# Performance work log

Measured on AMD Instinct MI355X. Metric: run time of the kernel, lower is better.

Reference implementation:

```python
import jax, jax.numpy as jnp
import numpy as np

N0, N1, N2, N3 = 262144, 65536, 16384, 4096
EPS = 1e-5  # BatchNorm1d default eps


def setup_inputs() -> dict:
    key = jax.random.key(0)
    ks = jax.random.split(key, 10)
    f0 = jax.random.normal(ks[0], (N0, 64), dtype=jnp.float32)
    f1 = jax.random.normal(ks[1], (N1, 128), dtype=jnp.float32)
    f2 = jax.random.normal(ks[2], (N2, 256), dtype=jnp.float32)
    f3 = jax.random.normal(ks[3], (N3, 512), dtype=jnp.float32)
    # upsampling indices: finer level gathers from coarser level
    idx0 = jax.random.randint(ks[4], (N2,), 0, N3, dtype=jnp.int32)   # f3 -> level2
    idx1 = jax.random.randint(ks[5], (N1,), 0, N2, dtype=jnp.int32)   # f2 -> level1
    idx2 = jax.random.randint(ks[6], (N0,), 0, N1, dtype=jnp.int32)   # f1 -> level0
    # BN weight init'd to constant 0.25 in the module; bias defaults to 0
    bn_w2, bn_b2 = jnp.full((512,), 0.25, jnp.float32), jnp.zeros((512,), jnp.float32)
    bn_w1, bn_b1 = jnp.full((256,), 0.25, jnp.float32), jnp.zeros((256,), jnp.float32)
    bn_w0, bn_b0 = jnp.full((128,), 0.25, jnp.float32), jnp.zeros((128,), jnp.float32)
    # Linear(in, out, bias=False) weights, torch layout [out, in]
    W2 = jax.random.normal(ks[7], (256, 512), dtype=jnp.float32) * 0.02
    W1 = jax.random.normal(ks[8], (128, 256), dtype=jnp.float32) * 0.02
    W0 = jax.random.normal(ks[9], (64, 128), dtype=jnp.float32) * 0.02
    return dict(f0=f0, f1=f1, f2=f2, f3=f3,
                bn_w2=bn_w2, bn_b2=bn_b2, W2=W2,
                bn_w1=bn_w1, bn_b1=bn_b1, W1=W1,
                bn_w0=bn_w0, bn_b0=bn_b0, W0=W0,
                idx0=idx0, idx1=idx1, idx2=idx2)


def _decode(f, bn_w, bn_b, W):
    # BatchNorm1d (training-mode batch stats, biased variance) -> Linear (no bias)
    mean = jnp.mean(f, axis=0)
    var = jnp.var(f, axis=0)
    xn = (f - mean) * jax.lax.rsqrt(var + EPS)
    return (xn * bn_w + bn_b) @ W.T  # [N, out_ch]


def reference(f0, f1, f2, f3, bn_w2, bn_b2, W2, bn_w1, bn_b1, W1,
              bn_w0, bn_b0, W0, idx0, idx1, idx2):
    # gather (upsample) -> BN -> Linear -> residual add, coarse to fine
    f2 = f2 + _decode(f3[idx0], bn_w2, bn_b2, W2)   # [N2, 256]
    f1 = f1 + _decode(f2[idx1], bn_w1, bn_b1, W1)   # [N1, 128]
    f0 = f0 + _decode(f1[idx2], bn_w0, bn_b0, W0)   # [N0, 64]
    return f0
```

## Files before the change

### kernel.cpp

```cpp
#include <hip/hip_runtime.h>
#include <hip/hip_cooperative_groups.h>

namespace cg = cooperative_groups;

#define BN_EPS 1e-5f

constexpr int PN0 = 262144, PN1 = 65536, PN2 = 16384, PN3 = 4096;
constexpr int NTHR = 512;
constexpr size_t MB = 1u << 20;

typedef __attribute__((ext_vector_type(8))) short short8;
typedef __attribute__((ext_vector_type(4))) float f32x4;
typedef __attribute__((ext_vector_type(4))) unsigned int u32x4;

__device__ __forceinline__ unsigned f2bf(float f) {
    unsigned u = __builtin_bit_cast(unsigned, f);
    u += 0x7fff + ((u >> 16) & 1);
    return u >> 16;
}
__device__ __forceinline__ float bf2f(unsigned h) {
    return __builtin_bit_cast(float, h << 16);
}
__device__ __forceinline__ f32x4 ntload4(const float* p) {
    return __builtin_nontemporal_load(reinterpret_cast<const f32x4*>(p));
}
__device__ __forceinline__ void ntstore4(float* p, f32x4 v) {
    __builtin_nontemporal_store(v, reinterpret_cast<f32x4*>(p));
}
#define SCHED_FENCE() __builtin_amdgcn_sched_barrier(0)

struct MegaArgs {
    const float *f0, *f1, *f2, *f3;
    const float *bnw2, *bnb2, *W2;
    const float *bnw1, *bnb1, *W1;
    const float *bnw0, *bnb0, *W0;
    const int *idx0, *idx1, *idx2;
    unsigned short *f3bf, *dec2, *dec1, *dec0, *f2p, *f1p;
    int *cnt2, *cnt1;
    float *part2, *part1, *part0;
    float *out;
};

template<int G, int NL>
__device__ __forceinline__ void red_write(float* aux, const float s[8], const float q[8],
                                          int t, int lr, int cgi,
                                          float* part, int vb, int C) {
    #pragma unroll
    for (int j = 0; j < 8; ++j) aux[(lr * G + cgi) * 8 + j] = s[j];
    __syncthreads();
    if (t < G) {
        float ss[8] = {};
        for (int l = 0; l < NL; ++l)
            #pragma unroll
            for (int j = 0; j < 8; ++j) ss[j] += aux[(l * G + t) * 8 + j];
        #pragma unroll
        for (int j = 0; j < 8; ++j)
            part[((size_t)vb * C + t * 8 + j) * 2] = ss[j];
    }
    __syncthreads();
    #pragma unroll
    for (int j = 0; j < 8; ++j) aux[(lr * G + cgi) * 8 + j] = q[j];
    __syncthreads();
    if (t < G) {
        float qq[8] = {};
        for (int l = 0; l < NL; ++l)
            #pragma unroll
            for (int j = 0; j < 8; ++j) qq[j] += aux[(l * G + t) * 8 + j];
        #pragma unroll
        for (int j = 0; j < 8; ++j)
            part[((size_t)vb * C + t * 8 + j) * 2 + 1] = qq[j];
    }
    __syncthreads();
}

__device__ void stats_gathered(const MegaArgs& a, int vb, int t, float* aux) {
    const int cgi = t & 63, lr = t >> 6;
    const int r0 = vb * 128;
    float s[8] = {}, q[8] = {};
    for (int ii = 0; ii < 4; ++ii) {
        int gi[8];
        #pragma unroll
        for (int j = 0; j < 8; ++j) gi[j] = a.idx0[r0 + lr + 4 * (ii * 8 + j)];
        float4 x0[8], x1[8];
        #pragma unroll
        for (int j = 0; j < 8; ++j) {
            const float* p = a.f3 + (size_t)gi[j] * 512 + cgi * 8;
            x0[j] = *reinterpret_cast<const float4*>(p);
            x1[j] = *reinterpret_cast<const float4*>(p + 4);
        }
        SCHED_FENCE();
        #pragma unroll
        for (int j = 0; j < 8; ++j) {
            float v[8] = {x0[j].x, x0[j].y, x0[j].z, x0[j].w,
                          x1[j].x, x1[j].y, x1[j].z, x1[j].w};
            #pragma unroll
            for (int k = 0; k < 8; ++k) { s[k] += v[k]; q[k] += v[k] * v[k]; }
        }
    }
    red_write<64, 4>(aux, s, q, t, lr, cgi, a.part2, vb, 512);
}

__device__ void cvt_f3(const MegaArgs& a, int vb, int t) {
    const int cgi = t & 63, lr = t >> 6;
    const int r0 = vb * 32;
    float4 x0[8], x1[8];
    #pragma unroll
    for (int i = 0; i < 8; ++i) {
        const float* p = a.f3 + (size_t)(r0 + lr + 4 * i) * 512 + cgi * 8;
        x0[i] = *reinterpret_cast<const float4*>(p);
        x1[i] = *reinterpret_cast<const float4*>(p + 4);
    }
    SCHED_FENCE();
    #pragma unroll
    for (int i = 0; i < 8; ++i) {
        uint4 o;
        o.x = f2bf(x0[i].x) | (f2bf(x0[i].y) << 16);
        o.y = f2bf(x0[i].z) | (f2bf(x0[i].w) << 16);
        o.z = f2bf(x1[i].x) | (f2bf(x1[i].y) << 16);
        o.w = f2bf(x1[i].z) | (f2bf(x1[i].w) << 16);
        *reinterpret_cast<uint4*>(a.f3bf + (size_t)(r0 + lr + 4 * i) * 512 + cgi * 8) = o;
    }
}

__device__ void phase1(const MegaArgs& a, int nbv, int vb0, int t, float* aux) {
    for (int vb = vb0; vb < 416; vb += nbv) {
        if (vb < 128) {
            stats_gathered(a, vb, t, aux);
        } else if (vb < 256) {
            cvt_f3(a, vb - 128, t);
        } else if (vb < 288) {
            int b = vb - 256;
            int v[8];
            #pragma unroll
            for (int i = 0; i < 8; ++i) v[i] = a.idx1[b * 2048 + i * 256 + t];
            SCHED_FENCE();
            #pragma unroll
            for (int i = 0; i < 8; ++i) atomicAdd(&a.cnt2[v[i]], 1);
        } else {
            int b = vb - 288;
            int v[8];
            #pragma unroll
            for (int i = 0; i < 8; ++i) v[i] = a.idx2[b * 2048 + i * 256 + t];
            SCHED_FENCE();
            #pragma unroll
            for (int i = 0; i < 8; ++i) atomicAdd(&a.cnt1[v[i]], 1);
        }
    }
}

template<int K, int NB>
__device__ void calc_scsh(int tid, const float* part, const float* bnw, const float* bnb,
                          float invN, float* sc, float* sh) {
    for (int c = tid; c < K; c += NTHR) {
        float s = 0.f, q = 0.f;
        for (int b = 0; b < NB; ++b) {
            float2 p = *reinterpret_cast<const float2*>(part + ((size_t)b * K + c) * 2);
            s += p.x;
            q += p.y;
        }
        float mean = s * invN;
        float var = fmaxf(q * invN - mean * mean, 0.f);
        float scl = bnw[c] * rsqrtf(var + BN_EPS);
        sc[c] = scl;
        sh[c] = bnb[c] - mean * scl;
    }
    __syncthreads();
}

__device__ void g2_phase(const MegaArgs& a, int nb, int bid, int tid,
                         unsigned short* Wl, float* sc, float* sh, float* dl) {
    constexpr int K = 512;
    calc_scsh<512, 128>(tid, a.part2, a.bnw2, a.bnb2, 1.f / PN2, sc, sh);
    const int lane = tid & 63;
    const int w = tid >> 6;
    const int l15 = lane & 15, lg = lane >> 4;
    const int n32 = tid >> 4, kc = tid & 15;

    for (int vb = bid; vb < 256; vb += nb) {
        const int chunk = vb & 31, panel = vb >> 5;
        const int row = chunk * 128 + w * 16 + l15;
        const unsigned short* xp = a.f3bf + (size_t)row * K + lg * 8;
        short8 xf[16];
        #pragma unroll
        for (int kk = 0; kk < 16; ++kk)
            xf[kk] = *reinterpret_cast<const short8*>(xp + kk * 32);

        {
            const float* wrow = a.W2 + (size_t)(panel * 32 + n32) * K;
            float dp = 0.f;
            #pragma unroll
            for (int i = 0; i < 4; ++i) {
                int k = kc * 32 + i * 8;
                float4 w0 = *reinterpret_cast<const float4*>(wrow + k);
                float4 w1 = *reinterpret_cast<const float4*>(wrow + k + 4);
                float4 s0 = *reinterpret_cast<const float4*>(&sc[k]);
                float4 s1 = *reinterpret_cast<const float4*>(&sc[k + 4]);
                float4 h0 = *reinterpret_cast<const float4*>(&sh[k]);
                float4 h1 = *reinterpret_cast<const float4*>(&sh[k + 4]);
                dp += h0.x * w0.x + h0.y * w0.y + h0.z * w0.z + h0.w * w0.w
                    + h1.x * w1.x + h1.y * w1.y + h1.z * w1.z + h1.w * w1.w;
                uint4 o;
                o.x = f2bf(w0.x * s0.x) | (f2bf(w0.y * s0.y) << 16);
                o.y = f2bf(w0.z * s0.z) | (f2bf(w0.w * s0.w) << 16);
                o.z = f2bf(w1.x * s1.x) | (f2bf(w1.y * s1.y) << 16);
                o.w = f2bf(w1.z * s1.z) | (f2bf(w1.w * s1.w) << 16);
                int si = (n32 * K + k) ^ ((n32 & 7) << 3);
                *reinterpret_cast<uint4*>(&Wl[si]) = o;
            }
            dp += __shfl_xor(dp, 1); dp += __shfl_xor(dp, 2);
            dp += __shfl_xor(dp, 4); dp += __shfl_xor(dp, 8);
            if (kc == 0) dl[n32] = dp;
        }
        __syncthreads();

        f32x4 acc[2];
        acc[0] = (f32x4){0.f, 0.f, 0.f, 0.f};
        acc[1] = (f32x4){0.f, 0.f, 0.f, 0.f};
        #pragma unroll
        for (int kk = 0; kk < 16; ++kk) {
            #pragma unroll
            for (int ni = 0; ni < 2; ++ni) {
                const int si = ((ni * 16 + l15) * K + kk * 32 + lg * 8) ^ ((l15 & 7) << 3);
                short8 wf = *reinterpret_cast<const short8*>(&Wl[si]);
                acc[ni] = __builtin_amdgcn_mfma_f32_16x16x32_bf16(wf, xf[kk], acc[ni], 0, 0, 0);
            }
        }

        const size_t rowoff = (size_t)row * 256 + panel * 32;
        #pragma unroll
        for (int ni = 0; ni < 2; ++ni) {
            float4 dr = *reinterpret_cast<const float4*>(&dl[ni * 16 + lg * 4]);
            size_t off = rowoff + ni * 16 + lg * 4;
            float v0 = dr.x + acc[ni][0];
            float v1 = dr.y + acc[ni][1];
            float v2 = dr.z + acc[ni][2];
            float v3 = dr.w + acc[ni][3];
            *reinterpret_cast<uint2*>(&a.dec2[off]) =
                make_uint2(f2bf(v0) | (f2bf(v1) << 16), f2bf(v2) | (f2bf(v3) << 16));
        }
        __syncthreads();
    }
}

__device__ void g1_phase(const MegaArgs& a, int nb, int bid, int tid,
                         unsigned short* Wl, float* sc, float* sh, float* dl) {
    constexpr int K = 256;
    calc_scsh<256, 256>(tid, a.part1, a.bnw1, a.bnb1, 1.f / PN1, sc, sh);
    const int lane = tid & 63;
    const int w = tid >> 6;
    const int l15 = lane & 15, lg = lane >> 4;
    const int n = tid >> 3, kc = tid & 7;

    for (int vb = bid; vb < 256; vb += nb) {
        const int chunk = vb & 127, panel = vb >> 7;
        const int row = chunk * 128 + w * 16 + l15;
        const unsigned short* xp = a.f2p + (size_t)row * K + lg * 8;
        short8 xf[8];
        #pragma unroll
        for (int kk = 0; kk < 8; ++kk)
            xf[kk] = *reinterpret_cast<const short8*>(xp + kk * 32);

        {
            const float* wrow = a.W1 + (size_t)(panel * 64 + n) * K;
            float dp = 0.f;
            #pragma unroll
            for (int i = 0; i < 4; ++i) {
                int k = kc * 32 + i * 8;
                float4 w0 = *reinterpret_cast<const float4*>(wrow + k);
                float4 w1 = *reinterpret_cast<const float4*>(wrow + k + 4);
                float4 s0 = *reinterpret_cast<const float4*>(&sc[k]);
                float4 s1 = *reinterpret_cast<const float4*>(&sc[k + 4]);
                float4 h0 = *reinterpret_cast<const float4*>(&sh[k]);
                float4 h1 = *reinterpret_cast<const float4*>(&sh[k + 4]);
                dp += h0.x * w0.x + h0.y * w0.y + h0.z * w0.z + h0.w * w0.w
                    + h1.x * w1.x + h1.y * w1.y + h1.z * w1.z + h1.w * w1.w;
                uint4 o;
                o.x = f2bf(w0.x * s0.x) | (f2bf(w0.y * s0.y) << 16);
                o.y = f2bf(w0.z * s0.z) | (f2bf(w0.w * s0.w) << 16);
                o.z = f2bf(w1.x * s1.x) | (f2bf(w1.y * s1.y) << 16);
                o.w = f2bf(w1.z * s1.z) | (f2bf(w1.w * s1.w) << 16);
                int si = (n * K + k) ^ ((n & 7) << 3);
                *reinterpret_cast<uint4*>(&Wl[si]) = o;
            }
            dp += __shfl_xor(dp, 1); dp += __shfl_xor(dp, 2); dp += __shfl_xor(dp, 4);
            if (kc == 0) dl[n] = dp;
        }
        __syncthreads();

        f32x4 acc[4];
        #pragma unroll
        for (int ni = 0; ni < 4; ++ni) acc[ni] = (f32x4){0.f, 0.f, 0.f, 0.f};
        #pragma unroll
        for (int kk = 0; kk < 8; ++kk) {
            #pragma unroll
            for (int ni = 0; ni < 4; ++ni) {
                const int si = ((ni * 16 + l15) * K + kk * 32 + lg * 8) ^ ((l15 & 7) << 3);
                short8 wf = *reinterpret_cast<const short8*>(&Wl[si]);
                acc[ni] = __builtin_amdgcn_mfma_f32_16x16x32_bf16(wf, xf[kk], acc[ni], 0, 0, 0);
            }
        }

        const size_t rowoff = (size_t)row * 128 + panel * 64;
        #pragma unroll
        for (int ni = 0; ni < 4; ++ni) {
            float4 dr = *reinterpret_cast<const float4*>(&dl[ni * 16 + lg * 4]);
            size_t off = rowoff + ni * 16 + lg * 4;
            float v0 = dr.x + acc[ni][0];
            float v1 = dr.y + acc[ni][1];
            float v2 = dr.z + acc[ni][2];
            float v3 = dr.w + acc[ni][3];
            *reinterpret_cast<uint2*>(&a.dec1[off]) =
                make_uint2(f2bf(v0) | (f2bf(v1) << 16), f2bf(v2) | (f2bf(v3) << 16));
        }
        __syncthreads();
    }
}

__device__ void g0_phase(const MegaArgs& a, int nb, int bid, int tid,
                         unsigned short* Wl, float* sc, float* sh, float* dl) {
    constexpr int K = 128;
    calc_scsh<128, 512>(tid, a.part0, a.bnw0, a.bnb0, 1.f / PN0, sc, sh);
    const int lane = tid & 63;
    const int w = tid >> 6;
    const int l15 = lane & 15, lg = lane >> 4;
    const int n = tid >> 3, kc = tid & 7;

    {
        const float* wrow = a.W0 + (size_t)n * K;
        float dp = 0.f;
        #pragma unroll
        for (int i = 0; i < 2; ++i) {
            int k = kc * 16 + i * 8;
            float4 w0 = *reinterpret_cast<const float4*>(wrow + k);
            float4 w1 = *reinterpret_cast<const float4*>(wrow + k + 4);
            float4 s0 = *reinterpret_cast<const float4*>(&sc[k]);
            float4 s1 = *reinterpret_cast<const float4*>(&sc[k + 4]);
            float4 h0 = *reinterpret_cast<const float4*>(&sh[k]);
            float4 h1 = *reinterpret_cast<const float4*>(&sh[k + 4]);
            dp += h0.x * w0.x + h0.y * w0.y + h0.z * w0.z + h0.w * w0.w
                + h1.x * w1.x + h1.y * w1.y + h1.z * w1.z + h1.w * w1.w;
            uint4 o;
            o.x = f2bf(w0.x * s0.x) | (f2bf(w0.y * s0.y) << 16);
            o.y = f2bf(w0.z * s0.z) | (f2bf(w0.w * s0.w) << 16);
            o.z = f2bf(w1.x * s1.x) | (f2bf(w1.y * s1.y) << 16);
            o.w = f2bf(w1.z * s1.z) | (f2bf(w1.w * s1.w) << 16);
            int si = (n * K + k) ^ ((n & 7) << 3);
            *reinterpret_cast<uint4*>(&Wl[si]) = o;
        }
        dp += __shfl_xor(dp, 1); dp += __shfl_xor(dp, 2); dp += __shfl_xor(dp, 4);
        if (kc == 0) dl[n] = dp;
    }
    __syncthreads();

    float4 dr[4];
    #pragma unroll
    for (int ni = 0; ni < 4; ++ni)
        dr[ni] = *reinterpret_cast<const float4*>(&dl[ni * 16 + lg * 4]);

    for (int vb = bid; vb < 2048; vb += nb) {
        const int row = vb * 128 + w * 16 + l15;
        const unsigned short* xp = a.f1p + (size_t)row * K + lg * 8;
        short8 xf[4];
        #pragma unroll
        for (int kk = 0; kk < 4; ++kk)
            xf[kk] = *reinterpret_cast<const short8*>(xp + kk * 32);
        f32x4 acc[4];
        #pragma unroll
        for (int ni = 0; ni < 4; ++ni) acc[ni] = (f32x4){0.f, 0.f, 0.f, 0.f};
        #pragma unroll
        for (int kk = 0; kk < 4; ++kk) {
            #pragma unroll
            for (int ni = 0; ni < 4; ++ni) {
                const int si = ((ni * 16 + l15) * K + kk * 32 + lg * 8) ^ ((l15 & 7) << 3);
                short8 wf = *reinterpret_cast<const short8*>(&Wl[si]);
                acc[ni] = __builtin_amdgcn_mfma_f32_16x16x32_bf16(wf, xf[kk], acc[ni], 0, 0, 0);
            }
        }
        const size_t rowoff = (size_t)row * 64;
        #pragma unroll
        for (int ni = 0; ni < 4; ++ni) {
            size_t off = rowoff + ni * 16 + lg * 4;
            float v0 = dr[ni].x + acc[ni][0];
            float v1 = dr[ni].y + acc[ni][1];
            float v2 = dr[ni].z + acc[ni][2];
            float v3 = dr[ni].w + acc[ni][3];
            *reinterpret_cast<uint2*>(&a.dec0[off]) =
                make_uint2(f2bf(v0) | (f2bf(v1) << 16), f2bf(v2) | (f2bf(v3) << 16));
        }
    }
}

template<int C, int IT, bool STATS, bool OUT_F32>
__device__ void ga_phase(int vb, int t, const float* base,
                         const unsigned short* dec, const int* idx,
                         const int* cnt_next, void* outv, float* part,
                         float* aux) {
    constexpr int G = C / 8;
    constexpr int NL = 256 / G;
    const int cgi = t % G;
    const int lr = t / G;
    const int r0 = vb * (NL * IT);

    int g[IT];
    #pragma unroll
    for (int i = 0; i < IT; ++i) g[i] = idx[r0 + lr + NL * i];

    float wreg[IT];
    if constexpr (STATS) {
        #pragma unroll
        for (int i = 0; i < IT; ++i) wreg[i] = (float)cnt_next[r0 + lr + NL * i];
    }

    u32x4 dv[IT];
    #pragma unroll
    for (int i = 0; i < IT; ++i)
        dv[i] = *reinterpret_cast<const u32x4*>(dec + (size_t)g[i] * C + cgi * 8);

    f32x4 b0[IT], b1[IT];
    #pragma unroll
    for (int i = 0; i < IT; ++i) {
        const float* bp = base + (size_t)(r0 + lr + NL * i) * C + cgi * 8;
        b0[i] = ntload4(bp);
        b1[i] = ntload4(bp + 4);
    }

    SCHED_FENCE();

    float s[8] = {}, q[8] = {};
    #pragma unroll
    for (int i = 0; i < IT; ++i) {
        const int r = r0 + lr + NL * i;
        float v[8];
        v[0] = b0[i][0] + bf2f(dv[i][0] & 0xffffu);
        v[1] = b0[i][1] + bf2f(dv[i][0] >> 16);
        v[2] = b0[i][2] + bf2f(dv[i][1] & 0xffffu);
        v[3] = b0[i][3] + bf2f(dv[i][1] >> 16);
        v[4] = b1[i][0] + bf2f(dv[i][2] & 0xffffu);
        v[5] = b1[i][1] + bf2f(dv[i][2] >> 16);
        v[6] = b1[i][2] + bf2f(dv[i][3] & 0xffffu);
        v[7] = b1[i][3] + bf2f(dv[i][3] >> 16);
        if constexpr (OUT_F32) {
            float* op = (float*)outv + (size_t)r * C + cgi * 8;
            ntstore4(op, (f32x4){v[0], v[1], v[2], v[3]});
            ntstore4(op + 4, (f32x4){v[4], v[5], v[6], v[7]});
        } else {
            unsigned h[8];
            #pragma unroll
            for (int j = 0; j < 8; ++j) h[j] = f2bf(v[j]);
            u32x4 o = {h[0] | (h[1] << 16), h[2] | (h[3] << 16),
                       h[4] | (h[5] << 16), h[6] | (h[7] << 16)};
            *reinterpret_cast<u32x4*>((unsigned short*)outv + (size_t)r * C + cgi * 8) = o;
            if constexpr (STATS) {
                #pragma unroll
                for (int j = 0; j < 8; ++j) {
                    float rv = bf2f(h[j]);
                    s[j] += wreg[i] * rv;
                    q[j] += wreg[i] * rv * rv;
                }
            }
        }
    }

    if constexpr (STATS)
        red_write<G, NL>(aux, s, q, t, lr, cgi, part, vb, C);
}

#define FENCE_SYNC { __threadfence(); gg.sync(); __threadfence(); }

__global__ __launch_bounds__(NTHR, 1) void mega(MegaArgs a) {
    __shared__ __align__(16) char smemA[32768];
    __shared__ float scshB[1088];
    cg::grid_group gg = cg::this_grid();
    const int nb = gridDim.x;
    const int bid = blockIdx.x;
    const int tid = threadIdx.x;
    const int h = tid >> 8, t = tid & 255;
    unsigned short* Wl = (unsigned short*)smemA;
    float* auxh = (float*)smemA + h * 2048;
    float* dl = scshB + 1024;

    phase1(a, nb * 2, bid * 2 + h, t, auxh);
    FENCE_SYNC;

    g2_phase(a, nb, bid, tid, Wl, scshB, scshB + 512, dl);
    FENCE_SYNC;

    for (int vb = bid * 2 + h; vb < 256; vb += nb * 2)
        ga_phase<256, 8, true, false>(vb, t, a.f2, a.dec2, a.idx0, a.cnt2, a.f2p, a.part1, auxh);
    FENCE_SYNC;

    g1_phase(a, nb, bid, tid, Wl, scshB, scshB + 256, dl);
    FENCE_SYNC;

    for (int vb = bid * 2 + h; vb < 512; vb += nb * 2)
        ga_phase<128, 8, true, false>(vb, t, a.f1, a.dec1, a.idx1, a.cnt1, a.f1p, a.part0, auxh);
    FENCE_SYNC;

    g0_phase(a, nb, bid, tid, Wl, scshB, scshB + 128, dl);
    FENCE_SYNC;

    for (int vb = bid * 2 + h; vb < 1024; vb += nb * 2)
        ga_phase<64, 8, false, true>(vb, t, a.f0, a.dec0, a.idx2, nullptr, a.out, nullptr, auxh);
}

__global__ __launch_bounds__(NTHR) void k_p1(MegaArgs a) {
    __shared__ float aux[4096];
    int h = threadIdx.x >> 8, t = threadIdx.x & 255;
    phase1(a, gridDim.x * 2, blockIdx.x * 2 + h, t, aux + h * 2048);
}
__global__ __launch_bounds__(NTHR) void k_g2(MegaArgs a) {
    __shared__ __align__(16) char smemA[32768];
    __shared__ float scshB[1088];
    g2_phase(a, gridDim.x, blockIdx.x, threadIdx.x, (unsigned short*)smemA,
             scshB, scshB + 512, scshB + 1024);
}
__global__ __launch_bounds__(NTHR) void k_g1(MegaArgs a) {
    __shared__ __align__(16) char smemA[32768];
    __shared__ float scshB[1088];
    g1_phase(a, gridDim.x, blockIdx.x, threadIdx.x, (unsigned short*)smemA,
             scshB, scshB + 256, scshB + 1024);
}
__global__ __launch_bounds__(NTHR) void k_g0(MegaArgs a) {
    __shared__ __align__(16) char smemA[16384];
    __shared__ float scshB[1088];
    g0_phase(a, gridDim.x, blockIdx.x, threadIdx.x, (unsigned short*)smemA,
             scshB, scshB + 128, scshB + 1024);
}
__global__ __launch_bounds__(NTHR) void k_a2(MegaArgs a) {
    __shared__ float aux[4096];
    int h = threadIdx.x >> 8, t = threadIdx.x & 255;
    for (int vb = blockIdx.x * 2 + h; vb < 256; vb += gridDim.x * 2)
        ga_phase<256, 8, true, false>(vb, t, a.f2, a.dec2, a.idx0, a.cnt2,
                                      a.f2p, a.part1, aux + h * 2048);
}
__global__ __launch_bounds__(NTHR) void k_a1(MegaArgs a) {
    __shared__ float aux[4096];
    int h = threadIdx.x >> 8, t = threadIdx.x & 255;
    for (int vb = blockIdx.x * 2 + h; vb < 512; vb += gridDim.x * 2)
        ga_phase<128, 8, true, false>(vb, t, a.f1, a.dec1, a.idx1, a.cnt1,
                                      a.f1p, a.part0, aux + h * 2048);
}
__global__ __launch_bounds__(NTHR) void k_a0(MegaArgs a) {
    int h = threadIdx.x >> 8, t = threadIdx.x & 255;
    for (int vb = blockIdx.x * 2 + h; vb < 1024; vb += gridDim.x * 2)
        ga_phase<64, 8, false, true>(vb, t, a.f0, a.dec0, a.idx2, nullptr,
                                     a.out, nullptr, nullptr);
}

extern "C" void kernel_launch(void* const* d_in, const int* in_sizes, int n_in,
                              void* d_out, int out_size, void* d_ws, size_t ws_size,
                              hipStream_t stream) {
    char* wsb = (char*)d_ws;
    unsigned short* f3bf = (unsigned short*)wsb;
    unsigned short* dec2 = (unsigned short*)(wsb + 4 * MB);
    unsigned short* dec1 = (unsigned short*)(wsb + 6 * MB);
    unsigned short* dec0 = (unsigned short*)(wsb + 10 * MB);
    unsigned short* f2p  = (unsigned short*)(wsb + 18 * MB);
    unsigned short* f1p  = (unsigned short*)(wsb + 26 * MB);
    int* cnt2 = (int*)(wsb + 42 * MB);
    int* cnt1 = cnt2 + PN2;
    float* part2 = (float*)(cnt1 + PN1);
    float* part1 = part2 + 128 * 512 * 2;
    float* part0 = part1 + 256 * 256 * 2;

    MegaArgs a;
    a.f0 = (const float*)d_in[0];
    a.f1 = (const float*)d_in[1];
    a.f2 = (const float*)d_in[2];
    a.f3 = (const float*)d_in[3];
    a.bnw2 = (const float*)d_in[4];
    a.bnb2 = (const float*)d_in[5];
    a.W2 = (const float*)d_in[6];
    a.bnw1 = (const float*)d_in[7];
    a.bnb1 = (const float*)d_in[8];
    a.W1 = (const float*)d_in[9];
    a.bnw0 = (const float*)d_in[10];
    a.bnb0 = (const float*)d_in[11];
    a.W0 = (const float*)d_in[12];
    a.idx0 = (const int*)d_in[13];
    a.idx1 = (const int*)d_in[14];
    a.idx2 = (const int*)d_in[15];
    a.f3bf = f3bf; a.dec2 = dec2; a.dec1 = dec1; a.dec0 = dec0;
    a.f2p = f2p; a.f1p = f1p;
    a.cnt2 = cnt2; a.cnt1 = cnt1;
    a.part2 = part2; a.part1 = part1; a.part0 = part0;
    a.out = (float*)d_out;

    hipMemsetAsync(cnt2, 0, (size_t)(PN2 + PN1) * sizeof(int), stream);

    int dev = 0;
    hipGetDevice(&dev);
    int coop = 0;
    hipDeviceGetAttribute(&coop, hipDeviceAttributeCooperativeLaunch, dev);
    int maxb = 0;
    hipOccupancyMaxActiveBlocksPerMultiprocessor(&maxb, mega, NTHR, 0);

    if (coop && maxb >= 1) {
        void* kargs[] = {&a};
        hipLaunchCooperativeKernel((void*)mega, dim3(256), dim3(NTHR), kargs, 0, stream);
    } else {
        k_p1<<<208, NTHR, 0, stream>>>(a);
        k_g2<<<256, NTHR, 0, stream>>>(a);
        k_a2<<<128, NTHR, 0, stream>>>(a);
        k_g1<<<256, NTHR, 0, stream>>>(a);
        k_a1<<<256, NTHR, 0, stream>>>(a);
        k_g0<<<256, NTHR, 0, stream>>>(a);
        k_a0<<<512, NTHR, 0, stream>>>(a);
    }
}
```

Measured before the change: 155.4 us.

## Replace cooperative megakernel with seven separate per-phase kernel launches

Drops the cooperative grid-synchronized megakernel and always launches seven specialized kernels, one block per work unit. Grid-wide barriers become kernel boundaries, and each kernel gets its own block size, launch bounds and shared-memory footprint so occupancy can rise. The trade is extra launch overhead and lost on-chip state between phases, in exchange for removing grid-sync stalls and the one-block-per-CU limit.

```diff
diff --git a/kernel.cpp b/kernel.cpp
--- a/kernel.cpp
+++ b/kernel.cpp
@@ -1,12 +1,8 @@
 #include <hip/hip_runtime.h>
-#include <hip/hip_cooperative_groups.h>
-
-namespace cg = cooperative_groups;
 
 #define BN_EPS 1e-5f
 
 constexpr int PN0 = 262144, PN1 = 65536, PN2 = 16384, PN3 = 4096;
-constexpr int NTHR = 512;
 constexpr size_t MB = 1u << 20;
 
 typedef __attribute__((ext_vector_type(8))) short short8;
@@ -70,88 +66,80 @@
         for (int j = 0; j < 8; ++j)
             part[((size_t)vb * C + t * 8 + j) * 2 + 1] = qq[j];
     }
-    __syncthreads();
-}
-
-__device__ void stats_gathered(const MegaArgs& a, int vb, int t, float* aux) {
-    const int cgi = t & 63, lr = t >> 6;
-    const int r0 = vb * 128;
-    float s[8] = {}, q[8] = {};
-    for (int ii = 0; ii < 4; ++ii) {
-        int gi[8];
-        #pragma unroll
-        for (int j = 0; j < 8; ++j) gi[j] = a.idx0[r0 + lr + 4 * (ii * 8 + j)];
-        float4 x0[8], x1[8];
-        #pragma unroll
-        for (int j = 0; j < 8; ++j) {
-            const float* p = a.f3 + (size_t)gi[j] * 512 + cgi * 8;
-            x0[j] = *reinterpret_cast<const float4*>(p);
-            x1[j] = *reinterpret_cast<const float4*>(p + 4);
-        }
-        SCHED_FENCE();
-        #pragma unroll
-        for (int j = 0; j < 8; ++j) {
-            float v[8] = {x0[j].x, x0[j].y, x0[j].z, x0[j].w,
-                          x1[j].x, x1[j].y, x1[j].z, x1[j].w};
+}
+
+__global__ __launch_bounds__(256, 4) void k_p1(MegaArgs a) {
+    __shared__ float aux[2048];
+    const int vb = blockIdx.x;
+    const int t = threadIdx.x;
+    if (vb < 128) {
+        const int cgi = t & 63, lr = t >> 6;
+        const int r0 = vb * 128;
+        float s[8] = {}, q[8] = {};
+        for (int ii = 0; ii < 4; ++ii) {
+            int gi[8];
             #pragma unroll
-            for (int k = 0; k < 8; ++k) { s[k] += v[k]; q[k] += v[k] * v[k]; }
-        }
-    }
-    red_write<64, 4>(aux, s, q, t, lr, cgi, a.part2, vb, 512);
-}
-
-__device__ void cvt_f3(const MegaArgs& a, int vb, int t) {
-    const int cgi = t & 63, lr = t >> 6;
-    const int r0 = vb * 32;
-    float4 x0[8], x1[8];
-    #pragma unroll
-    for (int i = 0; i < 8; ++i) {
-        const float* p = a.f3 + (size_t)(r0 + lr + 4 * i) * 512 + cgi * 8;
-        x0[i] = *reinterpret_cast<const float4*>(p);
-        x1[i] = *reinterpret_cast<const float4*>(p + 4);
-    }
-    SCHED_FENCE();
-    #pragma unroll
-    for (int i = 0; i < 8; ++i) {
-        uint4 o;
-        o.x = f2bf(x0[i].x) | (f2bf(x0[i].y) << 16);
-        o.y = f2bf(x0[i].z) | (f2bf(x0[i].w) << 16);
-        o.z = f2bf(x1[i].x) | (f2bf(x1[i].y) << 16);
-        o.w = f2bf(x1[i].z) | (f2bf(x1[i].w) << 16);
-        *reinterpret_cast<uint4*>(a.f3bf + (size_t)(r0 + lr + 4 * i) * 512 + cgi * 8) = o;
-    }
-}
-
-__device__ void phase1(const MegaArgs& a, int nbv, int vb0, int t, float* aux) {
-    for (int vb = vb0; vb < 416; vb += nbv) {
-        if (vb < 128) {
-            stats_gathered(a, vb, t, aux);
-        } else if (vb < 256) {
-            cvt_f3(a, vb - 128, t);
-        } else if (vb < 288) {
-            int b = vb - 256;
-            int v[8];
+            for (int j = 0; j < 8; ++j) gi[j] = a.idx0[r0 + lr + 4 * (ii * 8 + j)];
+            float4 x0[8], x1[8];
             #pragma unroll
-            for (int i = 0; i < 8; ++i) v[i] = a.idx1[b * 2048 + i * 256 + t];
+            for (int j = 0; j < 8; ++j) {
+                const float* p = a.f3 + (size_t)gi[j] * 512 + cgi * 8;
+                x0[j] = *reinterpret_cast<const float4*>(p);
+                x1[j] = *reinterpret_cast<const float4*>(p + 4);
+            }
             SCHED_FENCE();
             #pragma unroll
-            for (int i = 0; i < 8; ++i) atomicAdd(&a.cnt2[v[i]], 1);
-        } else {
-            int b = vb - 288;
-            int v[8];
-            #pragma unroll
-            for (int i = 0; i < 8; ++i) v[i] = a.idx2[b * 2048 + i * 256 + t];
-            SCHED_FENCE();
-            #pragma unroll
-            for (int i = 0; i < 8; ++i) atomicAdd(&a.cnt1[v[i]], 1);
-        }
-    }
-}
-
-template<int K, int NB>
+            for (int j = 0; j < 8; ++j) {
+                float v[8] = {x0[j].x, x0[j].y, x0[j].z, x0[j].w,
+                              x1[j].x, x1[j].y, x1[j].z, x1[j].w};
+                #pragma unroll
+                for (int k = 0; k < 8; ++k) { s[k] += v[k]; q[k] += v[k] * v[k]; }
+            }
+        }
+        red_write<64, 4>(aux, s, q, t, lr, cgi, a.part2, vb, 512);
+    } else if (vb < 256) {
+        const int cgi = t & 63, lr = t >> 6;
+        const int r0 = (vb - 128) * 32;
+        float4 x0[8], x1[8];
+        #pragma unroll
+        for (int i = 0; i < 8; ++i) {
+            const float* p = a.f3 + (size_t)(r0 + lr + 4 * i) * 512 + cgi * 8;
+            x0[i] = *reinterpret_cast<const float4*>(p);
+            x1[i] = *reinterpret_cast<const float4*>(p + 4);
+        }
+        SCHED_FENCE();
+        #pragma unroll
+        for (int i = 0; i < 8; ++i) {
+            uint4 o;
+            o.x = f2bf(x0[i].x) | (f2bf(x0[i].y) << 16);
+            o.y = f2bf(x0[i].z) | (f2bf(x0[i].w) << 16);
+            o.z = f2bf(x1[i].x) | (f2bf(x1[i].y) << 16);
+            o.w = f2bf(x1[i].z) | (f2bf(x1[i].w) << 16);
+            *reinterpret_cast<uint4*>(a.f3bf + (size_t)(r0 + lr + 4 * i) * 512 + cgi * 8) = o;
+        }
+    } else if (vb < 288) {
+        int b = vb - 256;
+        int v[8];
+        #pragma unroll
+        for (int i = 0; i < 8; ++i) v[i] = a.idx1[b * 2048 + i * 256 + t];
+        SCHED_FENCE();
+        #pragma unroll
+        for (int i = 0; i < 8; ++i) atomicAdd(&a.cnt2[v[i]], 1);
+    } else {
+        int b = vb - 288;
+        int v[8];
+        #pragma unroll
+        for (int i = 0; i < 8; ++i) v[i] = a.idx2[b * 2048 + i * 256 + t];
+        SCHED_FENCE();
+        #pragma unroll
+        for (int i = 0; i < 8; ++i) atomicAdd(&a.cnt1[v[i]], 1);
+    }
+}
+
+template<int K, int NB, int NT>
 __device__ void calc_scsh(int tid, const float* part, const float* bnw, const float* bnb,
                           float invN, float* sc, float* sh) {
-    for (int c = tid; c < K; c += NTHR) {
+    for (int c = tid; c < K; c += NT) {
         float s = 0.f, q = 0.f;
         for (int b = 0; b < NB; ++b) {
             float2 p = *reinterpret_cast<const float2*>(part + ((size_t)b * K + c) * 2);
@@ -167,159 +155,170 @@
     __syncthreads();
 }
 
-__device__ void g2_phase(const MegaArgs& a, int nb, int bid, int tid,
-                         unsigned short* Wl, float* sc, float* sh, float* dl) {
+__global__ __launch_bounds__(512, 4) void k_g2(MegaArgs a) {
     constexpr int K = 512;
-    calc_scsh<512, 128>(tid, a.part2, a.bnw2, a.bnb2, 1.f / PN2, sc, sh);
+    __shared__ __align__(16) unsigned short Wl[32 * 512];
+    __shared__ float scshB[1088];
+    float* sc = scshB;
+    float* sh = scshB + 512;
+    float* dl = scshB + 1024;
+    const int tid = threadIdx.x;
+    calc_scsh<512, 128, 512>(tid, a.part2, a.bnw2, a.bnb2, 1.f / PN2, sc, sh);
     const int lane = tid & 63;
     const int w = tid >> 6;
     const int l15 = lane & 15, lg = lane >> 4;
     const int n32 = tid >> 4, kc = tid & 15;
 
-    for (int vb = bid; vb < 256; vb += nb) {
-        const int chunk = vb & 31, panel = vb >> 5;
-        const int row = chunk * 128 + w * 16 + l15;
-        const unsigned short* xp = a.f3bf + (size_t)row * K + lg * 8;
-        short8 xf[16];
-        #pragma unroll
-        for (int kk = 0; kk < 16; ++kk)
-            xf[kk] = *reinterpret_cast<const short8*>(xp + kk * 32);
-
-        {
-            const float* wrow = a.W2 + (size_t)(panel * 32 + n32) * K;
-            float dp = 0.f;
-            #pragma unroll
-            for (int i = 0; i < 4; ++i) {
-                int k = kc * 32 + i * 8;
-                float4 w0 = *reinterpret_cast<const float4*>(wrow + k);
-                float4 w1 = *reinterpret_cast<const float4*>(wrow + k + 4);
-                float4 s0 = *reinterpret_cast<const float4*>(&sc[k]);
-                float4 s1 = *reinterpret_cast<const float4*>(&sc[k + 4]);
-                float4 h0 = *reinterpret_cast<const float4*>(&sh[k]);
-                float4 h1 = *reinterpret_cast<const float4*>(&sh[k + 4]);
-                dp += h0.x * w0.x + h0.y * w0.y + h0.z * w0.z + h0.w * w0.w
-                    + h1.x * w1.x + h1.y * w1.y + h1.z * w1.z + h1.w * w1.w;
-                uint4 o;
-                o.x = f2bf(w0.x * s0.x) | (f2bf(w0.y * s0.y) << 16);
-                o.y = f2bf(w0.z * s0.z) | (f2bf(w0.w * s0.w) << 16);
-                o.z = f2bf(w1.x * s1.x) | (f2bf(w1.y * s1.y) << 16);
-                o.w = f2bf(w1.z * s1.z) | (f2bf(w1.w * s1.w) << 16);
-                int si = (n32 * K + k) ^ ((n32 & 7) << 3);
-                *reinterpret_cast<uint4*>(&Wl[si]) = o;
-            }
-            dp += __shfl_xor(dp, 1); dp += __shfl_xor(dp, 2);
-            dp += __shfl_xor(dp, 4); dp += __shfl_xor(dp, 8);
-            if (kc == 0) dl[n32] = dp;
-        }
-        __syncthreads();
-
-        f32x4 acc[2];
-        acc[0] = (f32x4){0.f, 0.f, 0.f, 0.f};
-        acc[1] = (f32x4){0.f, 0.f, 0.f, 0.f};
-        #pragma unroll
-        for (int kk = 0; kk < 16; ++kk) {
-            #pragma unroll
-            for (int ni = 0; ni < 2; ++ni) {
-                const int si = ((ni * 16 + l15) * K + kk * 32 + lg * 8) ^ ((l15 & 7) << 3);
-                short8 wf = *reinterpret_cast<const short8*>(&Wl[si]);
-                acc[ni] = __builtin_amdgcn_mfma_f32_16x16x32_bf16(wf, xf[kk], acc[ni], 0, 0, 0);
-            }
-        }
-
-        const size_t rowoff = (size_t)row * 256 + panel * 32;
+    const int vb = blockIdx.x;
+    const int chunk = vb & 31, panel = vb >> 5;
+    const int row = chunk * 128 + w * 16 + l15;
+    const unsigned short* xp = a.f3bf + (size_t)row * K + lg * 8;
+    short8 xf[16];
+    #pragma unroll
+    for (int kk = 0; kk < 16; ++kk)
+        xf[kk] = *reinterpret_cast<const short8*>(xp + kk * 32);
+
+    {
+        const float* wrow = a.W2 + (size_t)(panel * 32 + n32) * K;
+        float dp = 0.f;
+        #pragma unroll
+        for (int i = 0; i < 4; ++i) {
+            int k = kc * 32 + i * 8;
+            float4 w0 = *reinterpret_cast<const float4*>(wrow + k);
+            float4 w1 = *reinterpret_cast<const float4*>(wrow + k + 4);
+            float4 s0 = *reinterpret_cast<const float4*>(&sc[k]);
+            float4 s1 = *reinterpret_cast<const float4*>(&sc[k + 4]);
+            float4 h0 = *reinterpret_cast<const float4*>(&sh[k]);
+            float4 h1 = *reinterpret_cast<const float4*>(&sh[k + 4]);
+            dp += h0.x * w0.x + h0.y * w0.y + h0.z * w0.z + h0.w * w0.w
+                + h1.x * w1.x + h1.y * w1.y + h1.z * w1.z + h1.w * w1.w;
+            uint4 o;
+            o.x = f2bf(w0.x * s0.x) | (f2bf(w0.y * s0.y) << 16);
+            o.y = f2bf(w0.z * s0.z) | (f2bf(w0.w * s0.w) << 16);
+            o.z = f2bf(w1.x * s1.x) | (f2bf(w1.y * s1.y) << 16);
+            o.w = f2bf(w1.z * s1.z) | (f2bf(w1.w * s1.w) << 16);
+            int si = (n32 * K + k) ^ ((n32 & 7) << 3);
+            *reinterpret_cast<uint4*>(&Wl[si]) = o;
+        }
+        dp += __shfl_xor(dp, 1); dp += __shfl_xor(dp, 2);
+        dp += __shfl_xor(dp, 4); dp += __shfl_xor(dp, 8);
+        if (kc == 0) dl[n32] = dp;
+    }
+    __syncthreads();
+
+    f32x4 acc[2];
+    acc[0] = (f32x4){0.f, 0.f, 0.f, 0.f};
+    acc[1] = (f32x4){0.f, 0.f, 0.f, 0.f};
+    #pragma unroll
+    for (int kk = 0; kk < 16; ++kk) {
         #pragma unroll
         for (int ni = 0; ni < 2; ++ni) {
-            float4 dr = *reinterpret_cast<const float4*>(&dl[ni * 16 + lg * 4]);
-            size_t off = rowoff + ni * 16 + lg * 4;
-            float v0 = dr.x + acc[ni][0];
-            float v1 = dr.y + acc[ni][1];
-            float v2 = dr.z + acc[ni][2];
-            float v3 = dr.w + acc[ni][3];
-            *reinterpret_cast<uint2*>(&a.dec2[off]) =
-                make_uint2(f2bf(v0) | (f2bf(v1) << 16), f2bf(v2) | (f2bf(v3) << 16));
-        }
-        __syncthreads();
-    }
-}
-
-__device__ void g1_phase(const MegaArgs& a, int nb, int bid, int tid,
-                         unsigned short* Wl, float* sc, float* sh, float* dl) {
+            const int si = ((ni * 16 + l15) * K + kk * 32 + lg * 8) ^ ((l15 & 7) << 3);
+            short8 wf = *reinterpret_cast<const short8*>(&Wl[si]);
+            acc[ni] = __builtin_amdgcn_mfma_f32_16x16x32_bf16(wf, xf[kk], acc[ni], 0, 0, 0);
+        }
+    }
+
+    const size_t rowoff = (size_t)row * 256 + panel * 32;
+    #pragma unroll
+    for (int ni = 0; ni < 2; ++ni) {
+        float4 dr = *reinterpret_cast<const float4*>(&dl[ni * 16 + lg * 4]);
+        size_t off = rowoff + ni * 16 + lg * 4;
+        float v0 = dr.x + acc[ni][0];
+        float v1 = dr.y + acc[ni][1];
+        float v2 = dr.z + acc[ni][2];
+        float v3 = dr.w + acc[ni][3];
+        *reinterpret_cast<uint2*>(&a.dec2[off]) =
+            make_uint2(f2bf(v0) | (f2bf(v1) << 16), f2bf(v2) | (f2bf(v3) << 16));
+    }
+}
+
+__global__ __launch_bounds__(512, 4) void k_g1(MegaArgs a) {
     constexpr int K = 256;
-    calc_scsh<256, 256>(tid, a.part1, a.bnw1, a.bnb1, 1.f / PN1, sc, sh);
+    __shared__ __align__(16) unsigned short Wl[64 * 256];
+    __shared__ float scshB[576];
+    float* sc = scshB;
+    float* sh = scshB + 256;
+    float* dl = scshB + 512;
+    const int tid = threadIdx.x;
+    calc_scsh<256, 256, 512>(tid, a.part1, a.bnw1, a.bnb1, 1.f / PN1, sc, sh);
     const int lane = tid & 63;
     const int w = tid >> 6;
     const int l15 = lane & 15, lg = lane >> 4;
     const int n = tid >> 3, kc = tid & 7;
 
-    for (int vb = bid; vb < 256; vb += nb) {
-        const int chunk = vb & 127, panel = vb >> 7;
-        const int row = chunk * 128 + w * 16 + l15;
-        const unsigned short* xp = a.f2p + (size_t)row * K + lg * 8;
-        short8 xf[8];
-        #pragma unroll
-        for (int kk = 0; kk < 8; ++kk)
-            xf[kk] = *reinterpret_cast<const short8*>(xp + kk * 32);
-
-        {
-            const float* wrow = a.W1 + (size_t)(panel * 64 + n) * K;
-            float dp = 0.f;
-            #pragma unroll
-            for (int i = 0; i < 4; ++i) {
-                int k = kc * 32 + i * 8;
-                float4 w0 = *reinterpret_cast<const float4*>(wrow + k);
-                float4 w1 = *reinterpret_cast<const float4*>(wrow + k + 4);
-                float4 s0 = *reinterpret_cast<const float4*>(&sc[k]);
-                float4 s1 = *reinterpret_cast<const float4*>(&sc[k + 4]);
-                float4 h0 = *reinterpret_cast<const float4*>(&sh[k]);
-                float4 h1 = *reinterpret_cast<const float4*>(&sh[k + 4]);
-                dp += h0.x * w0.x + h0.y * w0.y + h0.z * w0.z + h0.w * w0.w
-                    + h1.x * w1.x + h1.y * w1.y + h1.z * w1.z + h1.w * w1.w;
-                uint4 o;
-                o.x = f2bf(w0.x * s0.x) | (f2bf(w0.y * s0.y) << 16);
-                o.y = f2bf(w0.z * s0.z) | (f2bf(w0.w * s0.w) << 16);
-                o.z = f2bf(w1.x * s1.x) | (f2bf(w1.y * s1.y) << 16);
-                o.w = f2bf(w1.z * s1.z) | (f2bf(w1.w * s1.w) << 16);
-                int si = (n * K + k) ^ ((n & 7) << 3);
-                *reinterpret_cast<uint4*>(&Wl[si]) = o;
-            }
-            dp += __shfl_xor(dp, 1); dp += __shfl_xor(dp, 2); dp += __shfl_xor(dp, 4);
-            if (kc == 0) dl[n] = dp;
-        }
-        __syncthreads();
-
-        f32x4 acc[4];
-        #pragma unroll
-        for (int ni = 0; ni < 4; ++ni) acc[ni] = (f32x4){0.f, 0.f, 0.f, 0.f};
-        #pragma unroll
-        for (int kk = 0; kk < 8; ++kk) {
-            #pragma unroll
-            for (int ni = 0; ni < 4; ++ni) {
-                const int si = ((ni * 16 + l15) * K + kk * 32 + lg * 8) ^ ((l15 & 7) << 3);
-                short8 wf = *reinterpret_cast<const short8*>(&Wl[si]);
-                acc[ni] = __builtin_amdgcn_mfma_f32_16x16x32_bf16(wf, xf[kk], acc[ni], 0, 0, 0);
-            }
-        }
-
-        const size_t rowoff = (size_t)row * 128 + panel * 64;
+    const int vb = blockIdx.x;
+    const int chunk = vb & 127, panel = vb >> 7;
+    const int row = chunk * 128 + w * 16 + l15;
+    const unsigned short* xp = a.f2p + (size_t)row * K + lg * 8;
+    short8 xf[8];
+    #pragma unroll
+    for (int kk = 0; kk < 8; ++kk)
+        xf[kk] = *reinterpret_cast<const short8*>(xp + kk * 32);
+
+    {
+        const float* wrow = a.W1 + (size_t)(panel * 64 + n) * K;
+        float dp = 0.f;
+        #pragma unroll
+        for (int i = 0; i < 4; ++i) {
+            int k = kc * 32 + i * 8;
+            float4 w0 = *reinterpret_cast<const float4*>(wrow + k);
+            float4 w1 = *reinterpret_cast<const float4*>(wrow + k + 4);
+            float4 s0 = *reinterpret_cast<const float4*>(&sc[k]);
+            float4 s1 = *reinterpret_cast<const float4*>(&sc[k + 4]);
+            float4 h0 = *reinterpret_cast<const float4*>(&sh[k]);
+            float4 h1 = *reinterpret_cast<const float4*>(&sh[k + 4]);
+            dp += h0.x * w0.x + h0.y * w0.y + h0.z * w0.z + h0.w * w0.w
+                + h1.x * w1.x + h1.y * w1.y + h1.z * w1.z + h1.w * w1.w;
+            uint4 o;
+            o.x = f2bf(w0.x * s0.x) | (f2bf(w0.y * s0.y) << 16);
+            o.y = f2bf(w0.z * s0.z) | (f2bf(w0.w * s0.w) << 16);
+            o.z = f2bf(w1.x * s1.x) | (f2bf(w1.y * s1.y) << 16);
+            o.w = f2bf(w1.z * s1.z) | (f2bf(w1.w * s1.w) << 16);
+            int si = (n * K + k) ^ ((n & 7) << 3);
+            *reinterpret_cast<uint4*>(&Wl[si]) = o;
+        }
+        dp += __shfl_xor(dp, 1); dp += __shfl_xor(dp, 2); dp += __shfl_xor(dp, 4);
+        if (kc == 0) dl[n] = dp;
+    }
+    __syncthreads();
+
+    f32x4 acc[4];
+    #pragma unroll
+    for (int ni = 0; ni < 4; ++ni) acc[ni] = (f32x4){0.f, 0.f, 0.f, 0.f};
+    #pragma unroll
+    for (int kk = 0; kk < 8; ++kk) {
         #pragma unroll
         for (int ni = 0; ni < 4; ++ni) {
-            float4 dr = *reinterpret_cast<const float4*>(&dl[ni * 16 + lg * 4]);
-            size_t off = rowoff + ni * 16 + lg * 4;
-            float v0 = dr.x + acc[ni][0];
-            float v1 = dr.y + acc[ni][1];
-            float v2 = dr.z + acc[ni][2];
-            float v3 = dr.w + acc[ni][3];
-            *reinterpret_cast<uint2*>(&a.dec1[off]) =
-                make_uint2(f2bf(v0) | (f2bf(v1) << 16), f2bf(v2) | (f2bf(v3) << 16));
-        }
-        __syncthreads();
-    }
-}
-
-__device__ void g0_phase(const MegaArgs& a, int nb, int bid, int tid,
-                         unsigned short* Wl, float* sc, float* sh, float* dl) {
+            const int si = ((ni * 16 + l15) * K + kk * 32 + lg * 8) ^ ((l15 & 7) << 3);
+            short8 wf = *reinterpret_cast<const short8*>(&Wl[si]);
+            acc[ni] = __builtin_amdgcn_mfma_f32_16x16x32_bf16(wf, xf[kk], acc[ni], 0, 0, 0);
+        }
+    }
+
+    const size_t rowoff = (size_t)row * 128 + panel * 64;
+    #pragma unroll
+    for (int ni = 0; ni < 4; ++ni) {
+        float4 dr = *reinterpret_cast<const float4*>(&dl[ni * 16 + lg * 4]);
+        size_t off = rowoff + ni * 16 + lg * 4;
+        float v0 = dr.x + acc[ni][0];
+        float v1 = dr.y + acc[ni][1];
+        float v2 = dr.z + acc[ni][2];
+        float v3 = dr.w + acc[ni][3];
+        *reinterpret_cast<uint2*>(&a.dec1[off]) =
+            make_uint2(f2bf(v0) | (f2bf(v1) << 16), f2bf(v2) | (f2bf(v3) << 16));
+    }
+}
+
+__global__ __launch_bounds__(512, 4) void k_g0(MegaArgs a) {
     constexpr int K = 128;
-    calc_scsh<128, 512>(tid, a.part0, a.bnw0, a.bnb0, 1.f / PN0, sc, sh);
+    __shared__ __align__(16) unsigned short Wl[64 * 128];
+    __shared__ float scshB[320];
+    float* sc = scshB;
+    float* sh = scshB + 128;
+    float* dl = scshB + 256;
+    const int tid = threadIdx.x;
+    calc_scsh<128, 512, 512>(tid, a.part0, a.bnw0, a.bnb0, 1.f / PN0, sc, sh);
     const int lane = tid & 63;
     const int w = tid >> 6;
     const int l15 = lane & 15, lg = lane >> 4;
@@ -357,44 +356,43 @@
     for (int ni = 0; ni < 4; ++ni)
         dr[ni] = *reinterpret_cast<const float4*>(&dl[ni * 16 + lg * 4]);
 
-    for (int vb = bid; vb < 2048; vb += nb) {
-        const int row = vb * 128 + w * 16 + l15;
-        const unsigned short* xp = a.f1p + (size_t)row * K + lg * 8;
-        short8 xf[4];
-        #pragma unroll
-        for (int kk = 0; kk < 4; ++kk)
-            xf[kk] = *reinterpret_cast<const short8*>(xp + kk * 32);
-        f32x4 acc[4];
-        #pragma unroll
-        for (int ni = 0; ni < 4; ++ni) acc[ni] = (f32x4){0.f, 0.f, 0.f, 0.f};
-        #pragma unroll
-        for (int kk = 0; kk < 4; ++kk) {
-            #pragma unroll
-            for (int ni = 0; ni < 4; ++ni) {
-                const int si = ((ni * 16 + l15) * K + kk * 32 + lg * 8) ^ ((l15 & 7) << 3);
-                short8 wf = *reinterpret_cast<const short8*>(&Wl[si]);
-                acc[ni] = __builtin_amdgcn_mfma_f32_16x16x32_bf16(wf, xf[kk], acc[ni], 0, 0, 0);
-            }
-        }
-        const size_t rowoff = (size_t)row * 64;
+    const int vb = blockIdx.x;
+    const int row = vb * 128 + w * 16 + l15;
+    const unsigned short* xp = a.f1p + (size_t)row * K + lg * 8;
+    short8 xf[4];
+    #pragma unroll
+    for (int kk = 0; kk < 4; ++kk)
+        xf[kk] = *reinterpret_cast<const short8*>(xp + kk * 32);
+    f32x4 acc[4];
+    #pragma unroll
+    for (int ni = 0; ni < 4; ++ni) acc[ni] = (f32x4){0.f, 0.f, 0.f, 0.f};
+    #pragma unroll
+    for (int kk = 0; kk < 4; ++kk) {
         #pragma unroll
         for (int ni = 0; ni < 4; ++ni) {
-            size_t off = rowoff + ni * 16 + lg * 4;
-            float v0 = dr[ni].x + acc[ni][0];
-            float v1 = dr[ni].y + acc[ni][1];
-            float v2 = dr[ni].z + acc[ni][2];
-            float v3 = dr[ni].w + acc[ni][3];
-            *reinterpret_cast<uint2*>(&a.dec0[off]) =
-                make_uint2(f2bf(v0) | (f2bf(v1) << 16), f2bf(v2) | (f2bf(v3) << 16));
-        }
+            const int si = ((ni * 16 + l15) * K + kk * 32 + lg * 8) ^ ((l15 & 7) << 3);
+            short8 wf = *reinterpret_cast<const short8*>(&Wl[si]);
+            acc[ni] = __builtin_amdgcn_mfma_f32_16x16x32_bf16(wf, xf[kk], acc[ni], 0, 0, 0);
+        }
+    }
+    const size_t rowoff = (size_t)row * 64;
+    #pragma unroll
+    for (int ni = 0; ni < 4; ++ni) {
+        size_t off = rowoff + ni * 16 + lg * 4;
+        float v0 = dr[ni].x + acc[ni][0];
+        float v1 = dr[ni].y + acc[ni][1];
+        float v2 = dr[ni].z + acc[ni][2];
+        float v3 = dr[ni].w + acc[ni][3];
+        *reinterpret_cast<uint2*>(&a.dec0[off]) =
+            make_uint2(f2bf(v0) | (f2bf(v1) << 16), f2bf(v2) | (f2bf(v3) << 16));
     }
 }
 
 template<int C, int IT, bool STATS, bool OUT_F32>
-__device__ void ga_phase(int vb, int t, const float* base,
-                         const unsigned short* dec, const int* idx,
-                         const int* cnt_next, void* outv, float* part,
-                         float* aux) {
+__device__ void ga_body(int vb, int t, const float* base,
+                        const unsigned short* dec, const int* idx,
+                        const int* cnt_next, void* outv, float* part,
+                        float* aux) {
     constexpr int G = C / 8;
     constexpr int NL = 256 / G;
     const int cgi = t % G;
@@ -465,86 +463,19 @@
         red_write<G, NL>(aux, s, q, t, lr, cgi, part, vb, C);
 }
 
-#define FENCE_SYNC { __threadfence(); gg.sync(); __threadfence(); }
-
-__global__ __launch_bounds__(NTHR, 1) void mega(MegaArgs a) {
-    __shared__ __align__(16) char smemA[32768];
-    __shared__ float scshB[1088];
-    cg::grid_group gg = cg::this_grid();
-    const int nb = gridDim.x;
-    const int bid = blockIdx.x;
-    const int tid = threadIdx.x;
-    const int h = tid >> 8, t = tid & 255;
-    unsigned short* Wl = (unsigned short*)smemA;
-    float* auxh = (float*)smemA + h * 2048;
-    float* dl = scshB + 1024;
-
-    phase1(a, nb * 2, bid * 2 + h, t, auxh);
-    FENCE_SYNC;
-
-    g2_phase(a, nb, bid, tid, Wl, scshB, scshB + 512, dl);
-    FENCE_SYNC;
-
-    for (int vb = bid * 2 + h; vb < 256; vb += nb * 2)
-        ga_phase<256, 8, true, false>(vb, t, a.f2, a.dec2, a.idx0, a.cnt2, a.f2p, a.part1, auxh);
-    FENCE_SYNC;
-
-    g1_phase(a, nb, bid, tid, Wl, scshB, scshB + 256, dl);
-    FENCE_SYNC;
-
-    for (int vb = bid * 2 + h; vb < 512; vb += nb * 2)
-        ga_phase<128, 8, true, false>(vb, t, a.f1, a.dec1, a.idx1, a.cnt1, a.f1p, a.part0, auxh);
-    FENCE_SYNC;
-
-    g0_phase(a, nb, bid, tid, Wl, scshB, scshB + 128, dl);
-    FENCE_SYNC;
-
-    for (int vb = bid * 2 + h; vb < 1024; vb += nb * 2)
-        ga_phase<64, 8, false, true>(vb, t, a.f0, a.dec0, a.idx2, nullptr, a.out, nullptr, auxh);
-}
-
-__global__ __launch_bounds__(NTHR) void k_p1(MegaArgs a) {
-    __shared__ float aux[4096];
-    int h = threadIdx.x >> 8, t = threadIdx.x & 255;
-    phase1(a, gridDim.x * 2, blockIdx.x * 2 + h, t, aux + h * 2048);
-}
-__global__ __launch_bounds__(NTHR) void k_g2(MegaArgs a) {
-    __shared__ __align__(16) char smemA[32768];
-    __shared__ float scshB[1088];
-    g2_phase(a, gridDim.x, blockIdx.x, threadIdx.x, (unsigned short*)smemA,
-             scshB, scshB + 512, scshB + 1024);
-}
-__global__ __launch_bounds__(NTHR) void k_g1(MegaArgs a) {
-    __shared__ __align__(16) char smemA[32768];
-    __shared__ float scshB[1088];
-    g1_phase(a, gridDim.x, blockIdx.x, threadIdx.x, (unsigned short*)smemA,
-             scshB, scshB + 256, scshB + 1024);
-}
-__global__ __launch_bounds__(NTHR) void k_g0(MegaArgs a) {
-    __shared__ __align__(16) char smemA[16384];
-    __shared__ float scshB[1088];
-    g0_phase(a, gridDim.x, blockIdx.x, threadIdx.x, (unsigned short*)smemA,
-             scshB, scshB + 128, scshB + 1024);
-}
-__global__ __launch_bounds__(NTHR) void k_a2(MegaArgs a) {
-    __shared__ float aux[4096];
-    int h = threadIdx.x >> 8, t = threadIdx.x & 255;
-    for (int vb = blockIdx.x * 2 + h; vb < 256; vb += gridDim.x * 2)
-        ga_phase<256, 8, true, false>(vb, t, a.f2, a.dec2, a.idx0, a.cnt2,
-                                      a.f2p, a.part1, aux + h * 2048);
-}
-__global__ __launch_bounds__(NTHR) void k_a1(MegaArgs a) {
-    __shared__ float aux[4096];
-    int h = threadIdx.x >> 8, t = threadIdx.x & 255;
-    for (int vb = blockIdx.x * 2 + h; vb < 512; vb += gridDim.x * 2)
-        ga_phase<128, 8, true, false>(vb, t, a.f1, a.dec1, a.idx1, a.cnt1,
-                                      a.f1p, a.part0, aux + h * 2048);
-}
-__global__ __launch_bounds__(NTHR) void k_a0(MegaArgs a) {
-    int h = threadIdx.x >> 8, t = threadIdx.x & 255;
-    for (int vb = blockIdx.x * 2 + h; vb < 1024; vb += gridDim.x * 2)
-        ga_phase<64, 8, false, true>(vb, t, a.f0, a.dec0, a.idx2, nullptr,
-                                     a.out, nullptr, nullptr);
+__global__ __launch_bounds__(256, 4) void k_a2(MegaArgs a) {
+    __shared__ float aux[2048];
+    ga_body<256, 8, true, false>(blockIdx.x, threadIdx.x, a.f2, a.dec2, a.idx0, a.cnt2,
+                                 a.f2p, a.part1, aux);
+}
+__global__ __launch_bounds__(256, 4) void k_a1(MegaArgs a) {
+    __shared__ float aux[2048];
+    ga_body<128, 8, true, false>(blockIdx.x, threadIdx.x, a.f1, a.dec1, a.idx1, a.cnt1,
+                                 a.f1p, a.part0, aux);
+}
+__global__ __launch_bounds__(256, 4) void k_a0(MegaArgs a) {
+    ga_body<64, 8, false, true>(blockIdx.x, threadIdx.x, a.f0, a.dec0, a.idx2, nullptr,
+                                a.out, nullptr, nullptr);
 }
 
 extern "C" void kernel_launch(void* const* d_in, const int* in_sizes, int n_in,
@@ -588,23 +519,11 @@
 
     hipMemsetAsync(cnt2, 0, (size_t)(PN2 + PN1) * sizeof(int), stream);
 
-    int dev = 0;
-    hipGetDevice(&dev);
-    int coop = 0;
-    hipDeviceGetAttribute(&coop, hipDeviceAttributeCooperativeLaunch, dev);
-    int maxb = 0;
-    hipOccupancyMaxActiveBlocksPerMultiprocessor(&maxb, mega, NTHR, 0);
-
-    if (coop && maxb >= 1) {
-        void* kargs[] = {&a};
-        hipLaunchCooperativeKernel((void*)mega, dim3(256), dim3(NTHR), kargs, 0, stream);
-    } else {
-        k_p1<<<208, NTHR, 0, stream>>>(a);
-        k_g2<<<256, NTHR, 0, stream>>>(a);
-        k_a2<<<128, NTHR, 0, stream>>>(a);
-        k_g1<<<256, NTHR, 0, stream>>>(a);
-        k_a1<<<256, NTHR, 0, stream>>>(a);
-        k_g0<<<256, NTHR, 0, stream>>>(a);
-        k_a0<<<512, NTHR, 0, stream>>>(a);
-    }
-}
+    k_p1<<<416, 256, 0, stream>>>(a);
+    k_g2<<<256, 512, 0, stream>>>(a);
+    k_a2<<<256, 256, 0, stream>>>(a);
+    k_g1<<<256, 512, 0, stream>>>(a);
+    k_a1<<<512, 256, 0, stream>>>(a);
+    k_g0<<<512, 512, 0, stream>>>(a);
+    k_a0<<<1024, 256, 0, stream>>>(a);
+}
```

Result: slower. 163.9 us (+5.5%).
